# Optimization experiments

Hardware: AMD Instinct MI355X
Metric: run time of the kernel (lower is better)

Reference implementation:

```python
import jax, jax.numpy as jnp
import numpy as np

EPS = 1e-07
N, Q = 1368, 21
WS = [16, 32, 64]
ST = [4, 8, 16]
OC = [64, 128, 256]


def _num_pos(n, w, s):
    return int((n - w) / s - EPS) + 1


def setup_inputs() -> dict:
    key = jax.random.key(0)
    kx, k0, k1, k2 = jax.random.split(key, 4)
    B = 64
    x = jax.random.normal(kx, (B, Q, N), dtype=jnp.float32)
    ws = []
    for kk, (w, s, d) in zip([k0, k1, k2], zip(WS, ST, OC)):
        P = _num_pos(N, w, s)
        # xavier-style small init, shape (Nk, q*w) as in FilterbankLinear.weight
        scale = np.sqrt(2.0 / (Q * w + d)).astype(np.float32)
        ws.append(scale * jax.random.normal(kk, (d * P, Q * w), dtype=jnp.float32))
    return {"x": x, "w0": ws[0], "w1": ws[1], "w2": ws[2]}


def _filterbank_linear(x, W, w, s, d):
    # x: (B, q, N); W: (d*P, q*w)
    B, q, n = x.shape
    P = _num_pos(n, w, s)
    # window starts: j*s for j in range(P-1), last window anchored at n-w
    starts = np.concatenate([np.arange(P - 1) * s, np.array([n - w])])
    idx = starts[:, None] + np.arange(w)            # (P, w) static gather indices
    win = x[:, :, idx]                              # (B, q, P, w)
    win = jnp.transpose(win, (0, 2, 1, 3)).reshape(B, P, q * w)  # (B, P, q*w), channel-major like fbank
    h = jnp.einsum('bpf,pdf->bpd', win, W.reshape(P, d, q * w))
    return h.reshape(B, P * d)


def reference(x, w0, w1, w2):
    # FilterbankEdge.forward(x, sample=False): concat of each FilterbankLinear output
    outs = [
        _filterbank_linear(x, W, w, s, d)
        for W, (w, s, d) in zip([w0, w1, w2], zip(WS, ST, OC))
    ]
    return jnp.concatenate(outs, axis=-1)  # (B, 64000)
```

## Files before the change

### kernel.cpp

```cpp
#include <hip/hip_runtime.h>

#define QDIM 21
#define NDIM 1368
#define OUTSTRIDE 64000

typedef __attribute__((ext_vector_type(4))) float f32x4;
typedef __attribute__((ext_vector_type(8))) short bf16x8s;

static __device__ __forceinline__ unsigned short f2bf(float f) {
    unsigned int u = __float_as_uint(f);
    return (unsigned short)((u + 0x7FFFu + ((u >> 16) & 1u)) >> 16);
}

template<int WLOG2, int NTX, int D, int P, int S, int K>
__device__ __forceinline__ void fbk_body(const float* __restrict__ x,
                                         const float* __restrict__ W,
                                         float* __restrict__ out,
                                         int bid,
                                         unsigned short (*As)[72],
                                         unsigned short (*Bs)[72]) {
    constexpr int WWIN = 1 << WLOG2;
    constexpr int KTILES = (K + 63) / 64;

    const int n0 = (bid % NTX) * 64;
    const int p  = bid / NTX;
    const int start = (p == P - 1) ? (NDIM - WWIN) : p * S;

    const int tid  = threadIdx.x;
    const int wid  = tid >> 6;
    const int lane = tid & 63;
    const int wm = (wid >> 1) * 32;
    const int wn = (wid & 1) * 32;
    const int lr = lane & 15;
    const int kb = (lane >> 4) * 8;

    const float* Wp = W + (size_t)(p * D + n0) * K;

    f32x4 acc[2][2] = {};
    float4 va[4], vb[4];

    auto load_tile = [&](int kbase) {
        #pragma unroll
        for (int i = 0; i < 4; ++i) {
            int idx = tid + i * 256;
            int row = idx >> 4;
            int c4  = (idx & 15) * 4;
            int f = kbase + c4;
            if ((K % 64 == 0) || f < K) {
                int q = f >> WLOG2;
                int j = f & (WWIN - 1);
                va[i] = *(const float4*)(x + ((size_t)row * QDIM + q) * NDIM + start + j);
                vb[i] = *(const float4*)(Wp + (size_t)row * K + f);
            } else {
                va[i] = make_float4(0.f, 0.f, 0.f, 0.f);
                vb[i] = make_float4(0.f, 0.f, 0.f, 0.f);
            }
        }
    };
    auto store_tile = [&]() {
        #pragma unroll
        for (int i = 0; i < 4; ++i) {
            int idx = tid + i * 256;
            int row = idx >> 4;
            int c4  = (idx & 15) * 4;
            ushort4 ua, ub;
            ua.x = f2bf(va[i].x); ua.y = f2bf(va[i].y);
            ua.z = f2bf(va[i].z); ua.w = f2bf(va[i].w);
            ub.x = f2bf(vb[i].x); ub.y = f2bf(vb[i].y);
            ub.z = f2bf(vb[i].z); ub.w = f2bf(vb[i].w);
            *(ushort4*)(&As[row][c4]) = ua;
            *(ushort4*)(&Bs[row][c4]) = ub;
        }
    };

    load_tile(0);
    store_tile();
    __syncthreads();

    #pragma unroll 1
    for (int kt = 0; kt < KTILES; ++kt) {
        if (kt + 1 < KTILES) load_tile((kt + 1) * 64);
        #pragma unroll
        for (int kk = 0; kk < 2; ++kk) {
            int ko = kk * 32 + kb;
            bf16x8s a0 = *(const bf16x8s*)(&As[wm + lr][ko]);
            bf16x8s a1 = *(const bf16x8s*)(&As[wm + 16 + lr][ko]);
            bf16x8s b0 = *(const bf16x8s*)(&Bs[wn + lr][ko]);
            bf16x8s b1 = *(const bf16x8s*)(&Bs[wn + 16 + lr][ko]);
            acc[0][0] = __builtin_amdgcn_mfma_f32_16x16x32_bf16(a0, b0, acc[0][0], 0, 0, 0);
            acc[0][1] = __builtin_amdgcn_mfma_f32_16x16x32_bf16(a0, b1, acc[0][1], 0, 0, 0);
            acc[1][0] = __builtin_amdgcn_mfma_f32_16x16x32_bf16(a1, b0, acc[1][0], 0, 0, 0);
            acc[1][1] = __builtin_amdgcn_mfma_f32_16x16x32_bf16(a1, b1, acc[1][1], 0, 0, 0);
        }
        __syncthreads();
        if (kt + 1 < KTILES) store_tile();
        __syncthreads();
    }

    const int colbase = p * D + n0;
    #pragma unroll
    for (int mi = 0; mi < 2; ++mi) {
        #pragma unroll
        for (int ni = 0; ni < 2; ++ni) {
            int col = colbase + wn + ni * 16 + lr;
            int rbase = wm + mi * 16 + (lane >> 4) * 4;
            #pragma unroll
            for (int r = 0; r < 4; ++r) {
                out[(size_t)(rbase + r) * OUTSTRIDE + col] = acc[mi][ni][r];
            }
        }
    }
}

__global__ __launch_bounds__(256)
void fbk_fused(const float* __restrict__ x,  const float* __restrict__ w0,
               const float* __restrict__ w1, const float* __restrict__ w2,
               float* __restrict__ out) {
    __shared__ unsigned short As[64][72];
    __shared__ unsigned short Bs[64][72];
    const int bid = blockIdx.x;
    if (bid < 328) {
        fbk_body<6, 4, 256, 82, 16, 1344>(x, w2, out + 43008, bid, As, Bs);
    } else if (bid < 662) {
        fbk_body<5, 2, 128, 167, 8, 672>(x, w1, out + 21632, bid - 328, As, Bs);
    } else {
        fbk_body<4, 1, 64, 338, 4, 336>(x, w0, out, bid - 662, As, Bs);
    }
}

extern "C" void kernel_launch(void* const* d_in, const int* in_sizes, int n_in,
                              void* d_out, int out_size, void* d_ws, size_t ws_size,
                              hipStream_t stream) {
    const float* x  = (const float*)d_in[0];
    const float* w0 = (const float*)d_in[1];
    const float* w1 = (const float*)d_in[2];
    const float* w2 = (const float*)d_in[3];
    float* out = (float*)d_out;
    fbk_fused<<<dim3(1000), 256, 0, stream>>>(x, w0, w1, w2, out);
}
```

Baseline: 51.19 us.

## Load MFMA operands straight from global into registers, dropping LDS staging

```diff
diff --git a/kernel.cpp b/kernel.cpp
--- a/kernel.cpp
+++ b/kernel.cpp
@@ -12,15 +12,22 @@
     return (unsigned short)((u + 0x7FFFu + ((u >> 16) & 1u)) >> 16);
 }
 
+static __device__ __forceinline__ bf16x8s cvt8(const float* s) {
+    bf16x8s r;
+    #pragma unroll
+    for (int i = 0; i < 8; ++i) r[i] = (short)f2bf(s[i]);
+    return r;
+}
+
 template<int WLOG2, int NTX, int D, int P, int S, int K>
 __device__ __forceinline__ void fbk_body(const float* __restrict__ x,
                                          const float* __restrict__ W,
-                                         float* __restrict__ out,
-                                         int bid,
-                                         unsigned short (*As)[72],
-                                         unsigned short (*Bs)[72]) {
+                                         float* __restrict__ out, int bid) {
     constexpr int WWIN = 1 << WLOG2;
-    constexpr int KTILES = (K + 63) / 64;
+    constexpr int G = (K + 31) / 32;
+    constexpr bool TAIL = (K % 32) != 0;
+    constexpr int ADV_EO = (WLOG2 == 6) ? 32 : ((32 >> WLOG2) * NDIM);
+    constexpr int ADV_OE = (WLOG2 == 6) ? (NDIM - 32) : ((32 >> WLOG2) * NDIM);
 
     const int n0 = (bid % NTX) * 64;
     const int p  = bid / NTX;
@@ -34,68 +41,73 @@
     const int lr = lane & 15;
     const int kb = (lane >> 4) * 8;
 
-    const float* Wp = W + (size_t)(p * D + n0) * K;
+    const int q0 = kb >> WLOG2;
+    const int j0 = kb & (WWIN - 1);
 
+    const float* pA0 = x + ((size_t)(wm + lr) * QDIM + q0) * NDIM + start + j0;
+    const float* pA1 = pA0 + (size_t)16 * QDIM * NDIM;
+    const float* pB0 = W + (size_t)(p * D + n0 + wn + lr) * K + kb;
+    const float* pB1 = pB0 + (size_t)16 * K;
+
+    int fg = kb;
+
+    float a0A[8], a1A[8], b0A[8], b1A[8];
+    float a0B[8], a1B[8], b0B[8], b1B[8];
     f32x4 acc[2][2] = {};
-    float4 va[4], vb[4];
 
-    auto load_tile = [&](int kbase) {
-        #pragma unroll
-        for (int i = 0; i < 4; ++i) {
-            int idx = tid + i * 256;
-            int row = idx >> 4;
-            int c4  = (idx & 15) * 4;
-            int f = kbase + c4;
-            if ((K % 64 == 0) || f < K) {
-                int q = f >> WLOG2;
-                int j = f & (WWIN - 1);
-                va[i] = *(const float4*)(x + ((size_t)row * QDIM + q) * NDIM + start + j);
-                vb[i] = *(const float4*)(Wp + (size_t)row * K + f);
-            } else {
-                va[i] = make_float4(0.f, 0.f, 0.f, 0.f);
-                vb[i] = make_float4(0.f, 0.f, 0.f, 0.f);
-            }
-        }
-    };
-    auto store_tile = [&]() {
-        #pragma unroll
-        for (int i = 0; i < 4; ++i) {
-            int idx = tid + i * 256;
-            int row = idx >> 4;
-            int c4  = (idx & 15) * 4;
-            ushort4 ua, ub;
-            ua.x = f2bf(va[i].x); ua.y = f2bf(va[i].y);
-            ua.z = f2bf(va[i].z); ua.w = f2bf(va[i].w);
-            ub.x = f2bf(vb[i].x); ub.y = f2bf(vb[i].y);
-            ub.z = f2bf(vb[i].z); ub.w = f2bf(vb[i].w);
-            *(ushort4*)(&As[row][c4]) = ua;
-            *(ushort4*)(&Bs[row][c4]) = ub;
-        }
-    };
+#define ISSUE(SET, ADV)                                                      \
+    {                                                                        \
+        bool v_ = true;                                                      \
+        if constexpr (TAIL) v_ = (fg < K);                                   \
+        if (v_) {                                                            \
+            *(float4*)&a0##SET[0] = *(const float4*)(pA0);                   \
+            *(float4*)&a0##SET[4] = *(const float4*)(pA0 + 4);               \
+            *(float4*)&a1##SET[0] = *(const float4*)(pA1);                   \
+            *(float4*)&a1##SET[4] = *(const float4*)(pA1 + 4);               \
+            *(float4*)&b0##SET[0] = *(const float4*)(pB0);                   \
+            *(float4*)&b0##SET[4] = *(const float4*)(pB0 + 4);               \
+            *(float4*)&b1##SET[0] = *(const float4*)(pB1);                   \
+            *(float4*)&b1##SET[4] = *(const float4*)(pB1 + 4);               \
+        } else {                                                             \
+            _Pragma("unroll")                                                \
+            for (int z_ = 0; z_ < 8; ++z_) {                                 \
+                a0##SET[z_] = 0.f; a1##SET[z_] = 0.f;                        \
+                b0##SET[z_] = 0.f; b1##SET[z_] = 0.f;                        \
+            }                                                                \
+        }                                                                    \
+        pA0 += (ADV); pA1 += (ADV); pB0 += 32; pB1 += 32;                    \
+        if constexpr (TAIL) fg += 32;                                        \
+    }
 
-    load_tile(0);
-    store_tile();
-    __syncthreads();
+#define COMPUTE(SET)                                                         \
+    {                                                                        \
+        bf16x8s A0_ = cvt8(a0##SET), A1_ = cvt8(a1##SET);                    \
+        bf16x8s B0_ = cvt8(b0##SET), B1_ = cvt8(b1##SET);                    \
+        acc[0][0] = __builtin_amdgcn_mfma_f32_16x16x32_bf16(A0_, B0_, acc[0][0], 0, 0, 0); \
+        acc[0][1] = __builtin_amdgcn_mfma_f32_16x16x32_bf16(A0_, B1_, acc[0][1], 0, 0, 0); \
+        acc[1][0] = __builtin_amdgcn_mfma_f32_16x16x32_bf16(A1_, B0_, acc[1][0], 0, 0, 0); \
+        acc[1][1] = __builtin_amdgcn_mfma_f32_16x16x32_bf16(A1_, B1_, acc[1][1], 0, 0, 0); \
+    }
 
+    ISSUE(A, ADV_EO);
+    int g = 0;
     #pragma unroll 1
-    for (int kt = 0; kt < KTILES; ++kt) {
-        if (kt + 1 < KTILES) load_tile((kt + 1) * 64);
-        #pragma unroll
-        for (int kk = 0; kk < 2; ++kk) {
-            int ko = kk * 32 + kb;
-            bf16x8s a0 = *(const bf16x8s*)(&As[wm + lr][ko]);
-            bf16x8s a1 = *(const bf16x8s*)(&As[wm + 16 + lr][ko]);
-            bf16x8s b0 = *(const bf16x8s*)(&Bs[wn + lr][ko]);
-            bf16x8s b1 = *(const bf16x8s*)(&Bs[wn + 16 + lr][ko]);
-            acc[0][0] = __builtin_amdgcn_mfma_f32_16x16x32_bf16(a0, b0, acc[0][0], 0, 0, 0);
-            acc[0][1] = __builtin_amdgcn_mfma_f32_16x16x32_bf16(a0, b1, acc[0][1], 0, 0, 0);
-            acc[1][0] = __builtin_amdgcn_mfma_f32_16x16x32_bf16(a1, b0, acc[1][0], 0, 0, 0);
-            acc[1][1] = __builtin_amdgcn_mfma_f32_16x16x32_bf16(a1, b1, acc[1][1], 0, 0, 0);
-        }
-        __syncthreads();
-        if (kt + 1 < KTILES) store_tile();
-        __syncthreads();
+    for (; g + 2 < G; g += 2) {
+        ISSUE(B, ADV_OE);
+        COMPUTE(A);
+        ISSUE(A, ADV_EO);
+        COMPUTE(B);
     }
+    if (g + 1 < G) {
+        ISSUE(B, ADV_OE);
+        COMPUTE(A);
+        COMPUTE(B);
+    } else {
+        COMPUTE(A);
+    }
+
+#undef ISSUE
+#undef COMPUTE
 
     const int colbase = p * D + n0;
     #pragma unroll
@@ -112,19 +124,17 @@
     }
 }
 
-__global__ __launch_bounds__(256)
+__global__ __launch_bounds__(256, 4)
 void fbk_fused(const float* __restrict__ x,  const float* __restrict__ w0,
                const float* __restrict__ w1, const float* __restrict__ w2,
                float* __restrict__ out) {
-    __shared__ unsigned short As[64][72];
-    __shared__ unsigned short Bs[64][72];
     const int bid = blockIdx.x;
     if (bid < 328) {
-        fbk_body<6, 4, 256, 82, 16, 1344>(x, w2, out + 43008, bid, As, Bs);
+        fbk_body<6, 4, 256, 82, 16, 1344>(x, w2, out + 43008, bid);
     } else if (bid < 662) {
-        fbk_body<5, 2, 128, 167, 8, 672>(x, w1, out + 21632, bid - 328, As, Bs);
+        fbk_body<5, 2, 128, 167, 8, 672>(x, w1, out + 21632, bid - 328);
     } else {
-        fbk_body<4, 1, 64, 338, 4, 336>(x, w0, out, bid - 662, As, Bs);
+        fbk_body<4, 1, 64, 338, 4, 336>(x, w0, out, bid - 662);
     }
 }
 
```

Measured after the change: 85.59 us. +67.2%, slower.

## Double-buffer LDS tiles with two-stage register prefetch and 8-wide loads

Applied to the files above, without the earlier changes.

```diff
diff --git a/kernel.cpp b/kernel.cpp
--- a/kernel.cpp
+++ b/kernel.cpp
@@ -6,21 +6,28 @@
 
 typedef __attribute__((ext_vector_type(4))) float f32x4;
 typedef __attribute__((ext_vector_type(8))) short bf16x8s;
+typedef __attribute__((ext_vector_type(8))) unsigned short u16x8;
 
 static __device__ __forceinline__ unsigned short f2bf(float f) {
     unsigned int u = __float_as_uint(f);
     return (unsigned short)((u + 0x7FFFu + ((u >> 16) & 1u)) >> 16);
 }
 
+static __device__ __forceinline__ u16x8 cvt8f(float4 a, float4 b) {
+    u16x8 r;
+    r[0] = f2bf(a.x); r[1] = f2bf(a.y); r[2] = f2bf(a.z); r[3] = f2bf(a.w);
+    r[4] = f2bf(b.x); r[5] = f2bf(b.y); r[6] = f2bf(b.z); r[7] = f2bf(b.w);
+    return r;
+}
+
 template<int WLOG2, int NTX, int D, int P, int S, int K>
 __device__ __forceinline__ void fbk_body(const float* __restrict__ x,
                                          const float* __restrict__ W,
-                                         float* __restrict__ out,
-                                         int bid,
-                                         unsigned short (*As)[72],
-                                         unsigned short (*Bs)[72]) {
+                                         float* __restrict__ out, int bid,
+                                         unsigned short (*As)[64][72],
+                                         unsigned short (*Bs)[64][72]) {
     constexpr int WWIN = 1 << WLOG2;
-    constexpr int KTILES = (K + 63) / 64;
+    constexpr int G64 = (K + 63) / 64;
 
     const int n0 = (bid % NTX) * 64;
     const int p  = bid / NTX;
@@ -36,65 +43,85 @@
 
     const float* Wp = W + (size_t)(p * D + n0) * K;
 
-    f32x4 acc[2][2] = {};
-    float4 va[4], vb[4];
+    int srow[2], scol[2];
+    #pragma unroll
+    for (int i = 0; i < 2; ++i) {
+        int idx = tid + i * 256;
+        srow[i] = idx >> 3;
+        scol[i] = (idx & 7) * 8;
+    }
 
-    auto load_tile = [&](int kbase) {
+    struct Stage { float4 a[2][2]; float4 b[2][2]; };
+    Stage sA, sB;
+
+    auto LOADR = [&](Stage& Sg, int t) {
         #pragma unroll
-        for (int i = 0; i < 4; ++i) {
-            int idx = tid + i * 256;
-            int row = idx >> 4;
-            int c4  = (idx & 15) * 4;
-            int f = kbase + c4;
+        for (int i = 0; i < 2; ++i) {
+            int f = t * 64 + scol[i];
             if ((K % 64 == 0) || f < K) {
                 int q = f >> WLOG2;
                 int j = f & (WWIN - 1);
-                va[i] = *(const float4*)(x + ((size_t)row * QDIM + q) * NDIM + start + j);
-                vb[i] = *(const float4*)(Wp + (size_t)row * K + f);
+                const float* pa = x + ((size_t)srow[i] * QDIM + q) * NDIM + start + j;
+                const float* pb = Wp + (size_t)srow[i] * K + f;
+                Sg.a[i][0] = *(const float4*)pa;
+                Sg.a[i][1] = *(const float4*)(pa + 4);
+                Sg.b[i][0] = *(const float4*)pb;
+                Sg.b[i][1] = *(const float4*)(pb + 4);
             } else {
-                va[i] = make_float4(0.f, 0.f, 0.f, 0.f);
-                vb[i] = make_float4(0.f, 0.f, 0.f, 0.f);
+                Sg.a[i][0] = Sg.a[i][1] = make_float4(0.f, 0.f, 0.f, 0.f);
+                Sg.b[i][0] = Sg.b[i][1] = make_float4(0.f, 0.f, 0.f, 0.f);
             }
         }
+        __builtin_amdgcn_sched_barrier(0);
     };
-    auto store_tile = [&]() {
+
+    auto WRITEL = [&](int buf, const Stage& Sg) {
         #pragma unroll
-        for (int i = 0; i < 4; ++i) {
-            int idx = tid + i * 256;
-            int row = idx >> 4;
-            int c4  = (idx & 15) * 4;
-            ushort4 ua, ub;
-            ua.x = f2bf(va[i].x); ua.y = f2bf(va[i].y);
-            ua.z = f2bf(va[i].z); ua.w = f2bf(va[i].w);
-            ub.x = f2bf(vb[i].x); ub.y = f2bf(vb[i].y);
-            ub.z = f2bf(vb[i].z); ub.w = f2bf(vb[i].w);
-            *(ushort4*)(&As[row][c4]) = ua;
-            *(ushort4*)(&Bs[row][c4]) = ub;
+        for (int i = 0; i < 2; ++i) {
+            *(u16x8*)(&As[buf][srow[i]][scol[i]]) = cvt8f(Sg.a[i][0], Sg.a[i][1]);
+            *(u16x8*)(&Bs[buf][srow[i]][scol[i]]) = cvt8f(Sg.b[i][0], Sg.b[i][1]);
         }
     };
 
-    load_tile(0);
-    store_tile();
-    __syncthreads();
-
-    #pragma unroll 1
-    for (int kt = 0; kt < KTILES; ++kt) {
-        if (kt + 1 < KTILES) load_tile((kt + 1) * 64);
+    f32x4 acc[2][2] = {};
+    auto COMPUTE = [&](int buf) {
         #pragma unroll
         for (int kk = 0; kk < 2; ++kk) {
             int ko = kk * 32 + kb;
-            bf16x8s a0 = *(const bf16x8s*)(&As[wm + lr][ko]);
-            bf16x8s a1 = *(const bf16x8s*)(&As[wm + 16 + lr][ko]);
-            bf16x8s b0 = *(const bf16x8s*)(&Bs[wn + lr][ko]);
-            bf16x8s b1 = *(const bf16x8s*)(&Bs[wn + 16 + lr][ko]);
+            bf16x8s a0 = *(const bf16x8s*)(&As[buf][wm + lr][ko]);
+            bf16x8s a1 = *(const bf16x8s*)(&As[buf][wm + 16 + lr][ko]);
+            bf16x8s b0 = *(const bf16x8s*)(&Bs[buf][wn + lr][ko]);
+            bf16x8s b1 = *(const bf16x8s*)(&Bs[buf][wn + 16 + lr][ko]);
             acc[0][0] = __builtin_amdgcn_mfma_f32_16x16x32_bf16(a0, b0, acc[0][0], 0, 0, 0);
             acc[0][1] = __builtin_amdgcn_mfma_f32_16x16x32_bf16(a0, b1, acc[0][1], 0, 0, 0);
             acc[1][0] = __builtin_amdgcn_mfma_f32_16x16x32_bf16(a1, b0, acc[1][0], 0, 0, 0);
             acc[1][1] = __builtin_amdgcn_mfma_f32_16x16x32_bf16(a1, b1, acc[1][1], 0, 0, 0);
         }
+    };
+
+    LOADR(sA, 0);
+    LOADR(sB, 1);
+    WRITEL(0, sA);
+    __syncthreads();
+
+    #pragma unroll 1
+    for (int g = 0; g + 2 < G64; g += 2) {
+        LOADR(sA, g + 2);
+        COMPUTE(0);
+        WRITEL(1, sB);
         __syncthreads();
-        if (kt + 1 < KTILES) store_tile();
+        if (g + 3 < G64) LOADR(sB, g + 3);
+        COMPUTE(1);
+        WRITEL(0, sA);
         __syncthreads();
+    }
+    if constexpr ((G64 & 1) == 0) {
+        COMPUTE(0);
+        WRITEL(1, sB);
+        __syncthreads();
+        COMPUTE(1);
+    } else {
+        COMPUTE(0);
     }
 
     const int colbase = p * D + n0;
@@ -112,12 +139,12 @@
     }
 }
 
-__global__ __launch_bounds__(256)
+__global__ __launch_bounds__(256, 4)
 void fbk_fused(const float* __restrict__ x,  const float* __restrict__ w0,
                const float* __restrict__ w1, const float* __restrict__ w2,
                float* __restrict__ out) {
-    __shared__ unsigned short As[64][72];
-    __shared__ unsigned short Bs[64][72];
+    __shared__ unsigned short As[2][64][72];
+    __shared__ unsigned short Bs[2][64][72];
     const int bid = blockIdx.x;
     if (bid < 328) {
         fbk_body<6, 4, 256, 82, 16, 1344>(x, w2, out + 43008, bid, As, Bs);
```

Measured after the change: 55.60 us. 8.6% more time.

## Stage fp32 tiles via direct global-to-LDS loads with triple-buffered async pipeline

Applied to the files above, without the earlier changes.

```diff
diff --git a/kernel.cpp b/kernel.cpp
--- a/kernel.cpp
+++ b/kernel.cpp
@@ -6,21 +6,39 @@
 
 typedef __attribute__((ext_vector_type(4))) float f32x4;
 typedef __attribute__((ext_vector_type(8))) short bf16x8s;
+typedef __attribute__((ext_vector_type(4))) unsigned int u32x4;
 
-static __device__ __forceinline__ unsigned short f2bf(float f) {
-    unsigned int u = __float_as_uint(f);
-    return (unsigned short)((u + 0x7FFFu + ((u >> 16) & 1u)) >> 16);
+typedef __attribute__((address_space(1))) const unsigned int* gas_p;
+typedef __attribute__((address_space(3))) unsigned int* las_p;
+
+static __device__ __forceinline__ void gload16(const float* g, char* l) {
+    __builtin_amdgcn_global_load_lds((gas_p)(const void*)g, (las_p)(void*)l, 16, 0, 0);
+}
+
+static __device__ __forceinline__ unsigned int pk2(float lo, float hi) {
+    unsigned int a = __float_as_uint(lo) + 0x8000u;
+    unsigned int b = __float_as_uint(hi) + 0x8000u;
+    return __builtin_amdgcn_perm(b, a, 0x07060302);
+}
+
+static __device__ __forceinline__ bf16x8s pack8(float4 lo, float4 hi) {
+    u32x4 p;
+    p[0] = pk2(lo.x, lo.y);
+    p[1] = pk2(lo.z, lo.w);
+    p[2] = pk2(hi.x, hi.y);
+    p[3] = pk2(hi.z, hi.w);
+    return __builtin_bit_cast(bf16x8s, p);
 }
 
 template<int WLOG2, int NTX, int D, int P, int S, int K>
 __device__ __forceinline__ void fbk_body(const float* __restrict__ x,
                                          const float* __restrict__ W,
-                                         float* __restrict__ out,
-                                         int bid,
-                                         unsigned short (*As)[72],
-                                         unsigned short (*Bs)[72]) {
+                                         float* __restrict__ out, int bid,
+                                         char* ldsraw) {
     constexpr int WWIN = 1 << WLOG2;
-    constexpr int KTILES = (K + 63) / 64;
+    constexpr int G = (K + 31) / 32;
+    constexpr bool TAIL = (K % 32) != 0;
+    constexpr int FMAXC = (K - 4) & ~3;
 
     const int n0 = (bid % NTX) * 64;
     const int p  = bid / NTX;
@@ -32,69 +50,87 @@
     const int wm = (wid >> 1) * 32;
     const int wn = (wid & 1) * 32;
     const int lr = lane & 15;
-    const int kb = (lane >> 4) * 8;
+    const int hi = lane >> 4;
+    const int kb = hi * 8;
 
-    const float* Wp = W + (size_t)(p * D + n0) * K;
+    const int lrow = lane >> 3;
+    const int g4   = ((lane & 7) ^ lrow) * 4;
+    const int r0   = 16 * wid + lrow;
+    const float* xb0 = x + (size_t)r0 * QDIM * NDIM + start;
+    const float* Wp  = W + (size_t)(p * D + n0) * K;
+    const float* wb0 = Wp + (size_t)r0 * K;
+    const float* wb1 = wb0 + (size_t)8 * K;
+    const int wA = 2048 * wid;
+
+    auto STAGE = [&](int t, int sbase) {
+        int f = t * 32 + g4;
+        if constexpr (TAIL) f = (f > FMAXC) ? FMAXC : f;
+        int q = f >> WLOG2;
+        int j = f & (WWIN - 1);
+        const float* ga = xb0 + q * NDIM + j;
+        char* la = ldsraw + sbase + wA;
+        char* lb = ldsraw + sbase + 8192 + wA;
+        gload16(ga, la);
+        gload16(ga + (size_t)8 * QDIM * NDIM, la + 1024);
+        gload16(wb0 + f, lb);
+        gload16(wb1 + f, lb + 1024);
+    };
+
+    const int x7 = lr & 7;
+    const int c0 = ((hi * 2)     ^ x7) * 16;
+    const int c1 = ((hi * 2 + 1) ^ x7) * 16;
+    const int oA0 = (wm + lr) * 128;
+    const int oA1 = (wm + 16 + lr) * 128;
+    const int oB0 = 8192 + (wn + lr) * 128;
+    const int oB1 = 8192 + (wn + 16 + lr) * 128;
 
     f32x4 acc[2][2] = {};
-    float4 va[4], vb[4];
 
-    auto load_tile = [&](int kbase) {
-        #pragma unroll
-        for (int i = 0; i < 4; ++i) {
-            int idx = tid + i * 256;
-            int row = idx >> 4;
-            int c4  = (idx & 15) * 4;
-            int f = kbase + c4;
-            if ((K % 64 == 0) || f < K) {
-                int q = f >> WLOG2;
-                int j = f & (WWIN - 1);
-                va[i] = *(const float4*)(x + ((size_t)row * QDIM + q) * NDIM + start + j);
-                vb[i] = *(const float4*)(Wp + (size_t)row * K + f);
-            } else {
-                va[i] = make_float4(0.f, 0.f, 0.f, 0.f);
-                vb[i] = make_float4(0.f, 0.f, 0.f, 0.f);
+    STAGE(0, 0);
+    STAGE(1, 16384);
+
+    int cs = 0;
+    #pragma unroll 1
+    for (int t = 0; t < G; ++t) {
+        if (t + 1 < G) { asm volatile("s_waitcnt vmcnt(4)" ::: "memory"); }
+        else           { asm volatile("s_waitcnt vmcnt(0)" ::: "memory"); }
+        __builtin_amdgcn_sched_barrier(0);
+        __builtin_amdgcn_s_barrier();
+        __builtin_amdgcn_sched_barrier(0);
+
+        const char* sb = ldsraw + cs;
+        float4 a00 = *(const float4*)(sb + oA0 + c0);
+        float4 a01 = *(const float4*)(sb + oA0 + c1);
+        float4 a10 = *(const float4*)(sb + oA1 + c0);
+        float4 a11 = *(const float4*)(sb + oA1 + c1);
+        float4 b00 = *(const float4*)(sb + oB0 + c0);
+        float4 b01 = *(const float4*)(sb + oB0 + c1);
+        float4 b10 = *(const float4*)(sb + oB1 + c0);
+        float4 b11 = *(const float4*)(sb + oB1 + c1);
+
+        if constexpr (TAIL) {
+            if (t == G - 1 && kb >= (K & 31)) {
+                float4 z = make_float4(0.f, 0.f, 0.f, 0.f);
+                a00 = z; a01 = z; a10 = z; a11 = z;
             }
         }
-    };
-    auto store_tile = [&]() {
-        #pragma unroll
-        for (int i = 0; i < 4; ++i) {
-            int idx = tid + i * 256;
-            int row = idx >> 4;
-            int c4  = (idx & 15) * 4;
-            ushort4 ua, ub;
-            ua.x = f2bf(va[i].x); ua.y = f2bf(va[i].y);
-            ua.z = f2bf(va[i].z); ua.w = f2bf(va[i].w);
-            ub.x = f2bf(vb[i].x); ub.y = f2bf(vb[i].y);
-            ub.z = f2bf(vb[i].z); ub.w = f2bf(vb[i].w);
-            *(ushort4*)(&As[row][c4]) = ua;
-            *(ushort4*)(&Bs[row][c4]) = ub;
+
+        bf16x8s A0 = pack8(a00, a01);
+        bf16x8s A1 = pack8(a10, a11);
+        bf16x8s B0 = pack8(b00, b01);
+        bf16x8s B1 = pack8(b10, b11);
+
+        acc[0][0] = __builtin_amdgcn_mfma_f32_16x16x32_bf16(A0, B0, acc[0][0], 0, 0, 0);
+        acc[0][1] = __builtin_amdgcn_mfma_f32_16x16x32_bf16(A0, B1, acc[0][1], 0, 0, 0);
+        acc[1][0] = __builtin_amdgcn_mfma_f32_16x16x32_bf16(A1, B0, acc[1][0], 0, 0, 0);
+        acc[1][1] = __builtin_amdgcn_mfma_f32_16x16x32_bf16(A1, B1, acc[1][1], 0, 0, 0);
+
+        __builtin_amdgcn_sched_barrier(0);
+        if (t + 2 < G) {
+            int pb = (cs == 0) ? 32768 : cs - 16384;
+            STAGE(t + 2, pb);
         }
-    };
-
-    load_tile(0);
-    store_tile();
-    __syncthreads();
-
-    #pragma unroll 1
-    for (int kt = 0; kt < KTILES; ++kt) {
-        if (kt + 1 < KTILES) load_tile((kt + 1) * 64);
-        #pragma unroll
-        for (int kk = 0; kk < 2; ++kk) {
-            int ko = kk * 32 + kb;
-            bf16x8s a0 = *(const bf16x8s*)(&As[wm + lr][ko]);
-            bf16x8s a1 = *(const bf16x8s*)(&As[wm + 16 + lr][ko]);
-            bf16x8s b0 = *(const bf16x8s*)(&Bs[wn + lr][ko]);
-            bf16x8s b1 = *(const bf16x8s*)(&Bs[wn + 16 + lr][ko]);
-            acc[0][0] = __builtin_amdgcn_mfma_f32_16x16x32_bf16(a0, b0, acc[0][0], 0, 0, 0);
-            acc[0][1] = __builtin_amdgcn_mfma_f32_16x16x32_bf16(a0, b1, acc[0][1], 0, 0, 0);
-            acc[1][0] = __builtin_amdgcn_mfma_f32_16x16x32_bf16(a1, b0, acc[1][0], 0, 0, 0);
-            acc[1][1] = __builtin_amdgcn_mfma_f32_16x16x32_bf16(a1, b1, acc[1][1], 0, 0, 0);
-        }
-        __syncthreads();
-        if (kt + 1 < KTILES) store_tile();
-        __syncthreads();
+        cs = (cs == 32768) ? 0 : cs + 16384;
     }
 
     const int colbase = p * D + n0;
@@ -103,7 +139,7 @@
         #pragma unroll
         for (int ni = 0; ni < 2; ++ni) {
             int col = colbase + wn + ni * 16 + lr;
-            int rbase = wm + mi * 16 + (lane >> 4) * 4;
+            int rbase = wm + mi * 16 + hi * 4;
             #pragma unroll
             for (int r = 0; r < 4; ++r) {
                 out[(size_t)(rbase + r) * OUTSTRIDE + col] = acc[mi][ni][r];
@@ -112,19 +148,18 @@
     }
 }
 
-__global__ __launch_bounds__(256)
+__global__ __launch_bounds__(256, 3)
 void fbk_fused(const float* __restrict__ x,  const float* __restrict__ w0,
                const float* __restrict__ w1, const float* __restrict__ w2,
                float* __restrict__ out) {
-    __shared__ unsigned short As[64][72];
-    __shared__ unsigned short Bs[64][72];
+    __shared__ __align__(16) char ldsraw[49152];
     const int bid = blockIdx.x;
     if (bid < 328) {
-        fbk_body<6, 4, 256, 82, 16, 1344>(x, w2, out + 43008, bid, As, Bs);
+        fbk_body<6, 4, 256, 82, 16, 1344>(x, w2, out + 43008, bid, ldsraw);
     } else if (bid < 662) {
-        fbk_body<5, 2, 128, 167, 8, 672>(x, w1, out + 21632, bid - 328, As, Bs);
+        fbk_body<5, 2, 128, 167, 8, 672>(x, w1, out + 21632, bid - 328, ldsraw);
     } else {
-        fbk_body<4, 1, 64, 338, 4, 336>(x, w0, out, bid - 662, As, Bs);
+        fbk_body<4, 1, 64, 338, 4, 336>(x, w0, out, bid - 662, ldsraw);
     }
 }
 
```

New measurement: 53.23 us. 1.04x slower.
